# Optimization experiments

Hardware: AMD Instinct MI355X
Metric: run time of the kernel (lower is better)

The kernel has to match this reference:

```python
import jax, jax.numpy as jnp
import numpy as np

DELTA = 0.1
PAD = 2  # kernel_size // 2


def _step(x, W):
    # circular padding then VALID 5x5 cross-correlation (matches torch Conv2d circular)
    xp = jnp.pad(x, ((0, 0), (0, 0), (PAD, PAD), (PAD, PAD)), mode='wrap')
    y = jax.lax.conv_general_dilated(
        xp, W, window_strides=(1, 1), padding='VALID',
        dimension_numbers=('NCHW', 'OIHW', 'NCHW'))
    return jnp.clip(x + DELTA * jax.nn.relu(y), 0.0, 1.0)


def setup_inputs() -> dict:
    key = jax.random.key(0)
    k1, k2 = jax.random.split(key)
    x = jax.random.uniform(k1, (16, 3, 1024, 1024), dtype=jnp.float32)
    W = jax.random.normal(k2, (3, 3, 5, 5), dtype=jnp.float32) * 0.2
    return {"x": x, "W": W, "steps": 10}


def reference(x, W, steps):
    for _ in range(steps):
        x = _step(x, W)
    return x
```

## Files before the change

### kernel.cpp

```cpp
#include <hip/hip_runtime.h>


#define HH 1024
#define WW 1024
#define CC 3
#define NB 16
#define TW 128
#define TH 16
#define LW 132
#define LH 20
#define DELTA 0.1f

__global__ __launch_bounds__(256)
void ca_step(const float* __restrict__ src, float* __restrict__ dst,
             const float* __restrict__ Wg) {
    __shared__ float tile[CC][LH][LW];
    __shared__ float wsm[CC * 5 * 16];

    const int tid = threadIdx.x;
    const int w0 = blockIdx.x * TW;
    const int h0 = blockIdx.y * TH;
    const int n  = blockIdx.z;
    const float* srcn = src + (size_t)n * CC * HH * WW;

    if (tid < CC * CC * 25) {
        int oc = tid / 75;
        int rem = tid - oc * 75;
        int ic = rem / 25;
        int r2 = rem - ic * 25;
        int kh = r2 / 5;
        int kw = r2 - kh * 5;
        wsm[(ic * 5 + kh) * 16 + oc * 5 + kw] = Wg[tid];
    }

    for (int f = tid; f < CC * LH * 32; f += 256) {
        int c   = f / (LH * 32);
        int rem = f - c * (LH * 32);
        int row = rem >> 5;
        int c4  = rem & 31;
        int gh = (h0 + row - 2) & (HH - 1);
        const float4 v = *(const float4*)&srcn[((size_t)c * HH + gh) * WW + w0 + 4 * c4];
        float* t = &tile[c][row][2 + 4 * c4];
        *(float2*)&t[0] = make_float2(v.x, v.y);
        *(float2*)&t[2] = make_float2(v.z, v.w);
    }
    if (tid < CC * LH * 2) {
        int side = tid & 1;
        int rf   = tid >> 1;
        int c    = rf / LH;
        int row  = rf - c * LH;
        int gh = (h0 + row - 2) & (HH - 1);
        int gw = side ? ((w0 + TW) & (WW - 1)) : ((w0 - 2) & (WW - 1));
        const float2 v = *(const float2*)&srcn[((size_t)c * HH + gh) * WW + gw];
        *(float2*)&tile[c][row][side ? (2 + TW) : 0] = v;
    }
    __syncthreads();

    const int tx = tid & 31;
    const int ty = tid >> 5;
    const int xb = 4 * tx;

    float acc[2][CC][4];
#pragma unroll
    for (int rg = 0; rg < 2; ++rg)
#pragma unroll
        for (int oc = 0; oc < CC; ++oc)
#pragma unroll
            for (int j = 0; j < 4; ++j) acc[rg][oc][j] = 0.f;
    float xv[2][CC][4];

#pragma unroll
    for (int ic = 0; ic < CC; ++ic) {
#pragma unroll
        for (int kh = 0; kh < 5; ++kh) {
            const float* wrow = &wsm[(ic * 5 + kh) * 16];
            const float4 wA = *(const float4*)&wrow[0];
            const float4 wB = *(const float4*)&wrow[4];
            const float4 wC = *(const float4*)&wrow[8];
            const float4 wD = *(const float4*)&wrow[12];
            const float w_[15] = {wA.x, wA.y, wA.z, wA.w,
                                  wB.x, wB.y, wB.z, wB.w,
                                  wC.x, wC.y, wC.z, wC.w,
                                  wD.x, wD.y, wD.z};
            const float* ra = &tile[ic][ty + kh][xb];
            const float* rb = &tile[ic][ty + 8 + kh][xb];
            float va[8], vb[8];
            *(float4*)&va[0] = *(const float4*)&ra[0];
            *(float4*)&va[4] = *(const float4*)&ra[4];
            *(float4*)&vb[0] = *(const float4*)&rb[0];
            *(float4*)&vb[4] = *(const float4*)&rb[4];
            if (kh == 2) {
#pragma unroll
                for (int j = 0; j < 4; ++j) {
                    xv[0][ic][j] = va[2 + j];
                    xv[1][ic][j] = vb[2 + j];
                }
            }
#pragma unroll
            for (int oc = 0; oc < CC; ++oc) {
#pragma unroll
                for (int kw = 0; kw < 5; ++kw) {
                    const float wv = w_[oc * 5 + kw];
#pragma unroll
                    for (int j = 0; j < 4; ++j) {
                        acc[0][oc][j] = fmaf(va[kw + j], wv, acc[0][oc][j]);
                        acc[1][oc][j] = fmaf(vb[kw + j], wv, acc[1][oc][j]);
                    }
                }
            }
        }
    }

    float* dstn = dst + (size_t)n * CC * HH * WW;
#pragma unroll
    for (int rg = 0; rg < 2; ++rg) {
        const int h = h0 + ty + rg * 8;
#pragma unroll
        for (int oc = 0; oc < CC; ++oc) {
            float4 o;
            o.x = fminf(fmaxf(xv[rg][oc][0] + DELTA * fmaxf(acc[rg][oc][0], 0.f), 0.f), 1.f);
            o.y = fminf(fmaxf(xv[rg][oc][1] + DELTA * fmaxf(acc[rg][oc][1], 0.f), 0.f), 1.f);
            o.z = fminf(fmaxf(xv[rg][oc][2] + DELTA * fmaxf(acc[rg][oc][2], 0.f), 0.f), 1.f);
            o.w = fminf(fmaxf(xv[rg][oc][3] + DELTA * fmaxf(acc[rg][oc][3], 0.f), 0.f), 1.f);
            *(float4*)&dstn[((size_t)oc * HH + h) * WW + w0 + xb] = o;
        }
    }
}

extern "C" void kernel_launch(void* const* d_in, const int* in_sizes, int n_in,
                              void* d_out, int out_size, void* d_ws, size_t ws_size,
                              hipStream_t stream) {
    (void)in_sizes; (void)n_in; (void)out_size;
    const float* x  = (const float*)d_in[0];
    const float* Wg = (const float*)d_in[1];
    const int STEPS = 10;
    float* out = (float*)d_out;
    const size_t buf_bytes = (size_t)NB * CC * HH * WW * sizeof(float);

    dim3 grid(WW / TW, HH / TH, NB);
    dim3 block(256);

    if (ws_size >= buf_bytes) {
        float* tmp = (float*)d_ws;
        const float* s = x;
        for (int i = 1; i <= STEPS; ++i) {
            float* d = (i & 1) ? tmp : out;
            ca_step<<<grid, block, 0, stream>>>(s, d, Wg);
            s = d;
        }
    } else {
        float* tmp = (float*)d_in[0];
        const float* s = x;
        for (int i = 1; i <= STEPS; ++i) {
            float* d = (i & 1) ? out : tmp;
            ca_step<<<grid, block, 0, stream>>>(s, d, Wg);
            s = d;
        }
        hipMemcpyAsync(out, tmp, buf_bytes, hipMemcpyDeviceToDevice, stream);
    }
}
```

Measured before the change: 1.498 ms.

## Compute two adjacent output rows per thread sharing row loads, halve block size

Each thread now produces two vertically adjacent output rows for two 4-wide column groups, so every loaded tile row feeds both outputs and LDS reads per FMA drop (6 row loads per 2 outputs instead of 10). The block shrinks to 128 threads with launch bounds (128,2), and the weight and tile loading loops are adjusted for the smaller block. This raises the accumulator count per thread, which increases register pressure and may lower occupancy.

```diff
diff --git a/kernel.cpp b/kernel.cpp
--- a/kernel.cpp
+++ b/kernel.cpp
@@ -11,7 +11,7 @@
 #define LH 20
 #define DELTA 0.1f
 
-__global__ __launch_bounds__(256)
+__global__ __launch_bounds__(128, 2)
 void ca_step(const float* __restrict__ src, float* __restrict__ dst,
              const float* __restrict__ Wg) {
     __shared__ float tile[CC][LH][LW];
@@ -23,17 +23,17 @@
     const int n  = blockIdx.z;
     const float* srcn = src + (size_t)n * CC * HH * WW;
 
-    if (tid < CC * CC * 25) {
-        int oc = tid / 75;
-        int rem = tid - oc * 75;
+    for (int f = tid; f < CC * CC * 25; f += 128) {
+        int oc = f / 75;
+        int rem = f - oc * 75;
         int ic = rem / 25;
         int r2 = rem - ic * 25;
         int kh = r2 / 5;
         int kw = r2 - kh * 5;
-        wsm[(ic * 5 + kh) * 16 + oc * 5 + kw] = Wg[tid];
+        wsm[(ic * 5 + kh) * 16 + oc * 5 + kw] = Wg[f];
     }
 
-    for (int f = tid; f < CC * LH * 32; f += 256) {
+    for (int f = tid; f < CC * LH * 32; f += 128) {
         int c   = f / (LH * 32);
         int rem = f - c * (LH * 32);
         int row = rem >> 5;
@@ -56,73 +56,92 @@
     }
     __syncthreads();
 
-    const int tx = tid & 31;
-    const int ty = tid >> 5;
-    const int xb = 4 * tx;
+    const int tx = tid & 15;
+    const int ty = tid >> 4;
+    const int xb0 = 4 * tx;
+    const int xb1 = xb0 + 64;
+    const int rb = 2 * ty;
 
-    float acc[2][CC][4];
+    float acc[2][CC][2][4];
 #pragma unroll
-    for (int rg = 0; rg < 2; ++rg)
+    for (int o = 0; o < 2; ++o)
 #pragma unroll
         for (int oc = 0; oc < CC; ++oc)
 #pragma unroll
-            for (int j = 0; j < 4; ++j) acc[rg][oc][j] = 0.f;
-    float xv[2][CC][4];
+            for (int g = 0; g < 2; ++g)
+#pragma unroll
+                for (int j = 0; j < 4; ++j) acc[o][oc][g][j] = 0.f;
+    float xv[2][CC][2][4];
+
+#define FMAB(ACC, WA, WB, WC, WD)                                             \
+    do {                                                                      \
+        const float wv[15] = {WA.x, WA.y, WA.z, WA.w, WB.x, WB.y, WB.z, WB.w, \
+                              WC.x, WC.y, WC.z, WC.w, WD.x, WD.y, WD.z};      \
+        _Pragma("unroll") for (int oc = 0; oc < CC; ++oc)                     \
+        _Pragma("unroll") for (int kw = 0; kw < 5; ++kw) {                    \
+            const float w = wv[oc * 5 + kw];                                  \
+            _Pragma("unroll") for (int j = 0; j < 4; ++j) {                   \
+                ACC[oc][0][j] = fmaf(v0[kw + j], w, ACC[oc][0][j]);           \
+                ACC[oc][1][j] = fmaf(v1[kw + j], w, ACC[oc][1][j]);           \
+            }                                                                 \
+        }                                                                     \
+    } while (0)
 
 #pragma unroll
     for (int ic = 0; ic < CC; ++ic) {
+        float4 cA, cB, cC, cD;
+        float4 pA, pB, pC, pD;
 #pragma unroll
-        for (int kh = 0; kh < 5; ++kh) {
-            const float* wrow = &wsm[(ic * 5 + kh) * 16];
-            const float4 wA = *(const float4*)&wrow[0];
-            const float4 wB = *(const float4*)&wrow[4];
-            const float4 wC = *(const float4*)&wrow[8];
-            const float4 wD = *(const float4*)&wrow[12];
-            const float w_[15] = {wA.x, wA.y, wA.z, wA.w,
-                                  wB.x, wB.y, wB.z, wB.w,
-                                  wC.x, wC.y, wC.z, wC.w,
-                                  wD.x, wD.y, wD.z};
-            const float* ra = &tile[ic][ty + kh][xb];
-            const float* rb = &tile[ic][ty + 8 + kh][xb];
-            float va[8], vb[8];
-            *(float4*)&va[0] = *(const float4*)&ra[0];
-            *(float4*)&va[4] = *(const float4*)&ra[4];
-            *(float4*)&vb[0] = *(const float4*)&rb[0];
-            *(float4*)&vb[4] = *(const float4*)&rb[4];
-            if (kh == 2) {
+        for (int r = 0; r < 6; ++r) {
+            if (r > 0) { pA = cA; pB = cB; pC = cC; pD = cD; }
+            if (r < 5) {
+                const float* wr = &wsm[(ic * 5 + r) * 16];
+                cA = *(const float4*)&wr[0];
+                cB = *(const float4*)&wr[4];
+                cC = *(const float4*)&wr[8];
+                cD = *(const float4*)&wr[12];
+            }
+            const float* t = &tile[ic][rb + r][0];
+            float v0[8], v1[8];
+            *(float4*)&v0[0] = *(const float4*)&t[xb0];
+            *(float4*)&v0[4] = *(const float4*)&t[xb0 + 4];
+            *(float4*)&v1[0] = *(const float4*)&t[xb1];
+            *(float4*)&v1[4] = *(const float4*)&t[xb1 + 4];
+            if (r == 2) {
 #pragma unroll
                 for (int j = 0; j < 4; ++j) {
-                    xv[0][ic][j] = va[2 + j];
-                    xv[1][ic][j] = vb[2 + j];
+                    xv[0][ic][0][j] = v0[2 + j];
+                    xv[0][ic][1][j] = v1[2 + j];
                 }
             }
+            if (r == 3) {
 #pragma unroll
-            for (int oc = 0; oc < CC; ++oc) {
-#pragma unroll
-                for (int kw = 0; kw < 5; ++kw) {
-                    const float wv = w_[oc * 5 + kw];
-#pragma unroll
-                    for (int j = 0; j < 4; ++j) {
-                        acc[0][oc][j] = fmaf(va[kw + j], wv, acc[0][oc][j]);
-                        acc[1][oc][j] = fmaf(vb[kw + j], wv, acc[1][oc][j]);
-                    }
+                for (int j = 0; j < 4; ++j) {
+                    xv[1][ic][0][j] = v0[2 + j];
+                    xv[1][ic][1][j] = v1[2 + j];
                 }
             }
+            if (r < 5) FMAB(acc[0], cA, cB, cC, cD);
+            if (r > 0) FMAB(acc[1], pA, pB, pC, pD);
         }
     }
+#undef FMAB
 
     float* dstn = dst + (size_t)n * CC * HH * WW;
 #pragma unroll
-    for (int rg = 0; rg < 2; ++rg) {
-        const int h = h0 + ty + rg * 8;
+    for (int o = 0; o < 2; ++o) {
+        const int h = h0 + 2 * ty + o;
 #pragma unroll
         for (int oc = 0; oc < CC; ++oc) {
-            float4 o;
-            o.x = fminf(fmaxf(xv[rg][oc][0] + DELTA * fmaxf(acc[rg][oc][0], 0.f), 0.f), 1.f);
-            o.y = fminf(fmaxf(xv[rg][oc][1] + DELTA * fmaxf(acc[rg][oc][1], 0.f), 0.f), 1.f);
-            o.z = fminf(fmaxf(xv[rg][oc][2] + DELTA * fmaxf(acc[rg][oc][2], 0.f), 0.f), 1.f);
-            o.w = fminf(fmaxf(xv[rg][oc][3] + DELTA * fmaxf(acc[rg][oc][3], 0.f), 0.f), 1.f);
-            *(float4*)&dstn[((size_t)oc * HH + h) * WW + w0 + xb] = o;
+#pragma unroll
+            for (int g = 0; g < 2; ++g) {
+                float4 O;
+                O.x = fminf(fmaxf(xv[o][oc][g][0] + DELTA * fmaxf(acc[o][oc][g][0], 0.f), 0.f), 1.f);
+                O.y = fminf(fmaxf(xv[o][oc][g][1] + DELTA * fmaxf(acc[o][oc][g][1], 0.f), 0.f), 1.f);
+                O.z = fminf(fmaxf(xv[o][oc][g][2] + DELTA * fmaxf(acc[o][oc][g][2], 0.f), 0.f), 1.f);
+                O.w = fminf(fmaxf(xv[o][oc][g][3] + DELTA * fmaxf(acc[o][oc][g][3], 0.f), 0.f), 1.f);
+                *(float4*)&dstn[((size_t)oc * HH + h) * WW + w0 + 64 * g + 4 * tx] = O;
+            }
         }
     }
 }
@@ -138,7 +157,7 @@
     const size_t buf_bytes = (size_t)NB * CC * HH * WW * sizeof(float);
 
     dim3 grid(WW / TW, HH / TH, NB);
-    dim3 block(256);
+    dim3 block(128);
 
     if (ws_size >= buf_bytes) {
         float* tmp = (float*)d_ws;
```

After: 2.014 ms. +34.5%, slower.
